# Kernel tuning notes

Hardware: AMD Instinct MI355X
Metric: run time of the kernel (lower is better)

Reference implementation:

```python
import jax, jax.numpy as jnp
import numpy as np


def _prelu(y, a):
    # nn.PReLU() with a single learned slope parameter
    return jnp.where(y >= 0, y, a * y)


def _proj1x1(x, w, b, a):
    # 1x1 conv: [N,C,H,W] x [O,C] -> [N,O,H,W], then bias + PReLU
    y = jnp.einsum('nchw,oc->nohw', x, w) + b[None, :, None, None]
    return _prelu(y, a)


def setup_inputs() -> dict:
    key = jax.random.key(0)
    ks = jax.random.split(key, 10)
    C, RC = 128, 64
    x = jax.random.normal(ks[0], (2, C, 96, 96), dtype=jnp.float32)
    s1 = 1.0 / np.sqrt(C)
    w1 = jax.random.normal(ks[1], (RC, C), dtype=jnp.float32) * s1
    b1 = jax.random.normal(ks[2], (RC,), dtype=jnp.float32) * 0.01
    a1 = jnp.full((1,), 0.25, dtype=jnp.float32)
    w2 = jax.random.normal(ks[3], (RC, C), dtype=jnp.float32) * s1
    b2 = jax.random.normal(ks[4], (RC,), dtype=jnp.float32) * 0.01
    a2 = jnp.full((1,), 0.25, dtype=jnp.float32)
    wa = jax.random.normal(ks[5], (C, C), dtype=jnp.float32) * s1
    ba = jax.random.normal(ks[6], (C,), dtype=jnp.float32) * 0.01
    aa = jnp.full((1,), 0.25, dtype=jnp.float32)
    return {"x": x, "w1": w1, "b1": b1, "a1": a1,
            "w2": w2, "b2": b2, "a2": a2,
            "wa": wa, "ba": ba, "aa": aa}


def reference(x, w1, b1, a1, w2, b2, a2, wa, ba, aa):
    N, C, H, W = x.shape
    HW = H * W
    # [N, rc, HW]
    x_embed_1 = _proj1x1(x, w1, b1, a1).reshape(N, -1, HW)
    # [N, HW, rc]
    x_embed_2 = _proj1x1(x, w2, b2, a2).reshape(N, -1, HW).transpose(0, 2, 1)
    # [N, C, HW]
    x_assembly = _proj1x1(x, wa, ba, aa).reshape(N, -1, HW)
    # [N, HW, HW]; NOTE: no 1/sqrt(d) scaling, softmax over dim=1 (faithful to torch)
    score = jax.nn.softmax(jnp.einsum('nqc,ncK->nqK', x_embed_2, x_embed_1), axis=1)
    out = jnp.einsum('ncq,nqK->ncK', x_assembly, score)
    return out.reshape(N, C, H, W)
```

## Files before the change

kernel.cpp:

```cpp
#include <hip/hip_runtime.h>

#define HWp 9216
#define CD 128
#define RC 64
#define NB 2
#define KSPLIT 4
#define NSTEPS 72
#define LOG2E 1.4426950408889634f

#define E2F_NSTR 589824
#define AVF_NSTR 1179648

typedef short s16x8 __attribute__((ext_vector_type(8)));
typedef unsigned short u16x8 __attribute__((ext_vector_type(8)));
typedef float fx4 __attribute__((ext_vector_type(4)));

__device__ __forceinline__ unsigned short f2bf(float f) {
    union { float f; unsigned int u; } cv; cv.f = f;
    unsigned int u = cv.u;
    u += 0x7FFFu + ((u >> 16) & 1u);
    return (unsigned short)(u >> 16);
}

__device__ __forceinline__ float fexp2(float x) {
    float r; asm("v_exp_f32 %0, %1" : "=v"(r) : "v"(x)); return r;
}

__device__ __forceinline__ unsigned int cvt_pk_bf16(float lo, float hi) {
    unsigned int r; asm("v_cvt_pk_bf16_f32 %0, %1, %2" : "=v"(r) : "v"(lo), "v"(hi)); return r;
}

__device__ __forceinline__ const float* uniform_ptr(const float* p) {
    unsigned long long v = (unsigned long long)(uintptr_t)p;
    unsigned int lo = __builtin_amdgcn_readfirstlane((unsigned int)v);
    unsigned int hi = __builtin_amdgcn_readfirstlane((unsigned int)(v >> 32));
    return (const float*)(uintptr_t)(((unsigned long long)hi << 32) | lo);
}

__global__ __launch_bounds__(256) void proj_kernel(
    const float* __restrict__ x,
    const float* __restrict__ w1, const float* __restrict__ b1, const float* __restrict__ a1,
    const float* __restrict__ w2, const float* __restrict__ b2, const float* __restrict__ a2,
    const float* __restrict__ wa, const float* __restrict__ ba, const float* __restrict__ aa,
    unsigned short* __restrict__ e1, unsigned short* __restrict__ e2f,
    unsigned short* __restrict__ avf)
{
    const int n = blockIdx.y;
    const int p0 = blockIdx.x * 64;
    const int wv = threadIdx.x >> 6;
    const int lane = threadIdx.x & 63;
    const int p = p0 + lane;
    const int row0 = blockIdx.z * 32 + wv * 8;
    const float* __restrict__ xb = x + (size_t)n * CD * HWp;

    const float* W; const float* B; const float* A; int r0; int mode; float oscale = 1.0f;
    if (row0 < 64)       { W = w1; B = b1; A = a1; r0 = row0;       mode = 0; oscale = LOG2E; }
    else if (row0 < 128) { W = w2; B = b2; A = a2; r0 = row0 - 64;  mode = 1; }
    else                 { W = wa; B = ba; A = aa; r0 = row0 - 128; mode = 2; }
    W = uniform_ptr(W); B = uniform_ptr(B);
    const float slope = A[0];

    float acc[8];
#pragma unroll
    for (int j = 0; j < 8; ++j) acc[j] = B[r0 + j];

    float xr[2][32];
#pragma unroll
    for (int i = 0; i < 32; ++i) xr[0][i] = xb[(size_t)i * HWp + p];
#pragma unroll
    for (int cc = 0; cc < 4; ++cc) {
        const int cur = cc & 1;
        if (cc < 3) {
#pragma unroll
            for (int i = 0; i < 32; ++i)
                xr[cur ^ 1][i] = xb[(size_t)((cc + 1) * 32 + i) * HWp + p];
        }
#pragma unroll
        for (int j = 0; j < 8; ++j) {
            const float* Wr = W + (size_t)(r0 + j) * CD + cc * 32;
            float a = acc[j];
#pragma unroll
            for (int i = 0; i < 32; ++i) a = __builtin_fmaf(Wr[i], xr[cur][i], a);
            acc[j] = a;
        }
    }
#pragma unroll
    for (int j = 0; j < 8; ++j) {
        float v = acc[j];
        acc[j] = (v >= 0.f ? v : slope * v) * oscale;
    }
    if (mode == 0) {
        u16x8 s0;
#pragma unroll
        for (int j = 0; j < 8; ++j) s0[j] = f2bf(acc[j]);
        unsigned short* dst = e1 + ((size_t)n * HWp + p) * RC + r0;
        *(u16x8*)(dst) = s0;
    } else if (mode == 1) {
        u16x8 s0;
#pragma unroll
        for (int j = 0; j < 8; ++j) s0[j] = f2bf(acc[j]);
        const int kb = p >> 5, kk = p & 31;
        const int l15w = ((kk >> 3) << 2) | (kk & 3);
        const int hw = (kk >> 2) & 1;
        const int ch = r0 >> 5;
        const int gA = (r0 >> 3) & 3;
        unsigned short* dst = e2f + (size_t)n * E2F_NSTR
                            + ((size_t)((kb * 4 + hw * 2 + ch) * 64 + gA * 16 + l15w)) * 8;
        *(u16x8*)(dst) = s0;
    } else {
        const int kb = p >> 5, gw = (p >> 3) & 3, jj = p & 7;
        const int ct = r0 >> 4;
        const int lbase = r0 & 15;
        unsigned short* base = avf + (size_t)n * AVF_NSTR
                             + ((size_t)((kb * 8 + ct) * 64 + gw * 16)) * 8 + jj;
#pragma unroll
        for (int j = 0; j < 8; ++j)
            base[(lbase + j) * 8] = f2bf(acc[j]);
    }
}

__global__ __launch_bounds__(256, 1) void attn_kernel(
    const unsigned short* __restrict__ e1,
    const unsigned short* __restrict__ e2f,
    const unsigned short* __restrict__ avf,
    float* __restrict__ out)
{
    const int wv = threadIdx.x >> 6;
    const int lane = threadIdx.x & 63;
    const int g = lane >> 4;
    const int l15 = lane & 15;

    const int bid = blockIdx.x;
    const int xcd = bid & 7;
    const int n = xcd >> 2;
    const int qslot = (xcd & 3) * 72 + (bid >> 3);
    const int qb = qslot * 32;

    const unsigned short* __restrict__ E1 = e1 + (size_t)n * HWp * RC;
    const unsigned short* __restrict__ E2F = e2f + (size_t)n * E2F_NSTR;
    const unsigned short* __restrict__ AVF = avf + (size_t)n * AVF_NSTR;

    s16x8 qf[2][2];
#pragma unroll
    for (int qc = 0; qc < 2; ++qc)
#pragma unroll
        for (int ch = 0; ch < 2; ++ch)
            qf[qc][ch] = *(const s16x8*)(E1 + ((size_t)(qb + qc * 16 + l15)) * RC + ch * 32 + g * 8);

    s16x8 ones;
#pragma unroll
    for (int j = 0; j < 8; ++j) ones[j] = (short)0x3F80;

    fx4 oacc[2][8];
    fx4 lacc[2];
#pragma unroll
    for (int qc = 0; qc < 2; ++qc) {
        lacc[qc] = (fx4){0.f, 0.f, 0.f, 0.f};
#pragma unroll
        for (int ct = 0; ct < 8; ++ct) oacc[qc][ct] = (fx4){0.f, 0.f, 0.f, 0.f};
    }

    const int kb0 = wv * NSTEPS;

    const unsigned short* kfp = E2F + (size_t)kb0 * 2048 + (size_t)lane * 8;
    const unsigned short* afp = AVF + (size_t)kb0 * 4096 + (size_t)lane * 8;

    s16x8 kfc[2][2];
#pragma unroll
    for (int h = 0; h < 2; ++h)
#pragma unroll
        for (int ch = 0; ch < 2; ++ch)
            kfc[h][ch] = *(const s16x8*)(kfp + (h * 2 + ch) * 512);
    kfp += 2048;

    union { s16x8 v; unsigned int w[4]; } pf[2];

    for (int kt = 0; kt < NSTEPS; ++kt) {
        s16x8 af[8];
#pragma unroll
        for (int ct = 0; ct < 8; ++ct)
            af[ct] = *(const s16x8*)(afp + ct * 512);
        afp += 4096;

        const unsigned short* kfsrc = (kt + 1 < NSTEPS) ? kfp : (kfp - 2048);
        s16x8 kfn[2][2];
#pragma unroll
        for (int h = 0; h < 2; ++h)
#pragma unroll
            for (int ch = 0; ch < 2; ++ch)
                kfn[h][ch] = *(const s16x8*)(kfsrc + (h * 2 + ch) * 512);
        kfp += 2048;

        fx4 s[2][2];
#pragma unroll
        for (int qc = 0; qc < 2; ++qc)
#pragma unroll
            for (int h = 0; h < 2; ++h) {
                fx4 a = (fx4){0.f, 0.f, 0.f, 0.f};
                a = __builtin_amdgcn_mfma_f32_16x16x32_bf16(kfc[h][0], qf[qc][0], a, 0, 0, 0);
                a = __builtin_amdgcn_mfma_f32_16x16x32_bf16(kfc[h][1], qf[qc][1], a, 0, 0, 0);
                s[qc][h] = a;
            }

#pragma unroll
        for (int qc = 0; qc < 2; ++qc) {
            float p0 = fexp2(s[qc][0][0]);
            float p1 = fexp2(s[qc][0][1]);
            float p2 = fexp2(s[qc][0][2]);
            float p3 = fexp2(s[qc][0][3]);
            float p4 = fexp2(s[qc][1][0]);
            float p5 = fexp2(s[qc][1][1]);
            float p6 = fexp2(s[qc][1][2]);
            float p7 = fexp2(s[qc][1][3]);
            pf[qc].w[0] = cvt_pk_bf16(p0, p1);
            pf[qc].w[1] = cvt_pk_bf16(p2, p3);
            pf[qc].w[2] = cvt_pk_bf16(p4, p5);
            pf[qc].w[3] = cvt_pk_bf16(p6, p7);
            lacc[qc] = __builtin_amdgcn_mfma_f32_16x16x32_bf16(ones, pf[qc].v, lacc[qc], 0, 0, 0);
        }

#pragma unroll
        for (int ct = 0; ct < 8; ++ct) {
            oacc[0][ct] = __builtin_amdgcn_mfma_f32_16x16x32_bf16(af[ct], pf[0].v, oacc[0][ct], 0, 0, 0);
            oacc[1][ct] = __builtin_amdgcn_mfma_f32_16x16x32_bf16(af[ct], pf[1].v, oacc[1][ct], 0, 0, 0);
        }

#pragma unroll
        for (int h = 0; h < 2; ++h)
#pragma unroll
            for (int ch = 0; ch < 2; ++ch)
                kfc[h][ch] = kfn[h][ch];
    }

    __shared__ float OA[32][CD + 4];
    __shared__ float LL[KSPLIT][32];
    __shared__ float LG[32];

    if (g == 0) {
#pragma unroll
        for (int qc = 0; qc < 2; ++qc)
            LL[wv][qc * 16 + l15] = lacc[qc][0];
    }
    __syncthreads();
    if (threadIdx.x < 32) {
        int q = threadIdx.x;
        float ls = 0.f;
#pragma unroll
        for (int w = 0; w < KSPLIT; ++w) ls += LL[w][q];
        LG[q] = ls;
    }
    for (int w = 0; w < KSPLIT; ++w) {
        if (wv == w) {
#pragma unroll
            for (int qc = 0; qc < 2; ++qc)
#pragma unroll
                for (int ct = 0; ct < 8; ++ct)
#pragma unroll
                    for (int r = 0; r < 4; ++r) {
                        int q = qc * 16 + l15;
                        int c = ct * 16 + g * 4 + r;
                        float v = oacc[qc][ct][r];
                        if (w == 0) OA[q][c] = v; else OA[q][c] += v;
                    }
        }
        __syncthreads();
    }
    {
        const int c = threadIdx.x >> 1;
        const int qh = (threadIdx.x & 1) * 16;
        float* __restrict__ dst = out + ((size_t)n * CD + c) * HWp + qb + qh;
#pragma unroll
        for (int j = 0; j < 16; ++j) dst[j] = OA[qh + j][c] / LG[qh + j];
    }
}

extern "C" void kernel_launch(void* const* d_in, const int* in_sizes, int n_in,
                              void* d_out, int out_size, void* d_ws, size_t ws_size,
                              hipStream_t stream) {
    const float* x  = (const float*)d_in[0];
    const float* w1 = (const float*)d_in[1];
    const float* b1 = (const float*)d_in[2];
    const float* a1 = (const float*)d_in[3];
    const float* w2 = (const float*)d_in[4];
    const float* b2 = (const float*)d_in[5];
    const float* a2 = (const float*)d_in[6];
    const float* wa = (const float*)d_in[7];
    const float* ba = (const float*)d_in[8];
    const float* aa = (const float*)d_in[9];
    float* out = (float*)d_out;

    char* ws = (char*)d_ws;
    unsigned short* e1  = (unsigned short*)ws;
    unsigned short* e2f = (unsigned short*)(ws + 2359296);
    unsigned short* avf = (unsigned short*)(ws + 4718592);

    dim3 pg(HWp / 64, NB, 8);
    proj_kernel<<<pg, 256, 0, stream>>>(x, w1, b1, a1, w2, b2, a2, wa, ba, aa, e1, e2f, avf);
    attn_kernel<<<dim3(576), 256, 0, stream>>>(e1, e2f, avf, out);
}
```

Measured before the change: 199.9 us.

## Retile attention blocks to 64 queries by half the channels

Each attention block now covers 64 queries and 64 output channels (a channel-group index is derived from the XCD id) instead of 32 queries and all 128 channels. The same number of value-tile loads now feeds twice as many query tiles, but the QK^T and exp work is duplicated across the two channel groups. Shared memory tiles and the output write mapping are resized to match. The projection kernel also drops its double-buffered x register prefetch for a simpler per-chunk load, which lowers register pressure.

```diff
diff --git a/kernel.cpp b/kernel.cpp
--- a/kernel.cpp
+++ b/kernel.cpp
@@ -63,24 +63,16 @@
     float acc[8];
 #pragma unroll
     for (int j = 0; j < 8; ++j) acc[j] = B[r0 + j];
-
-    float xr[2][32];
-#pragma unroll
-    for (int i = 0; i < 32; ++i) xr[0][i] = xb[(size_t)i * HWp + p];
-#pragma unroll
     for (int cc = 0; cc < 4; ++cc) {
-        const int cur = cc & 1;
-        if (cc < 3) {
-#pragma unroll
-            for (int i = 0; i < 32; ++i)
-                xr[cur ^ 1][i] = xb[(size_t)((cc + 1) * 32 + i) * HWp + p];
-        }
+        float xr[32];
+#pragma unroll
+        for (int i = 0; i < 32; ++i) xr[i] = xb[(size_t)(cc * 32 + i) * HWp + p];
 #pragma unroll
         for (int j = 0; j < 8; ++j) {
             const float* Wr = W + (size_t)(r0 + j) * CD + cc * 32;
             float a = acc[j];
 #pragma unroll
-            for (int i = 0; i < 32; ++i) a = __builtin_fmaf(Wr[i], xr[cur][i], a);
+            for (int i = 0; i < 32; ++i) a = __builtin_fmaf(Wr[i], xr[i], a);
             acc[j] = a;
         }
     }
@@ -133,16 +125,18 @@
     const int bid = blockIdx.x;
     const int xcd = bid & 7;
     const int n = xcd >> 2;
-    const int qslot = (xcd & 3) * 72 + (bid >> 3);
-    const int qb = qslot * 32;
+    const int cg = (xcd >> 1) & 1;
+    const int sub = xcd & 1;
+    const int qslot = (bid >> 3) * 2 + sub;
+    const int qb = qslot * 64;
 
     const unsigned short* __restrict__ E1 = e1 + (size_t)n * HWp * RC;
     const unsigned short* __restrict__ E2F = e2f + (size_t)n * E2F_NSTR;
     const unsigned short* __restrict__ AVF = avf + (size_t)n * AVF_NSTR;
 
-    s16x8 qf[2][2];
-#pragma unroll
-    for (int qc = 0; qc < 2; ++qc)
+    s16x8 qf[4][2];
+#pragma unroll
+    for (int qc = 0; qc < 4; ++qc)
 #pragma unroll
         for (int ch = 0; ch < 2; ++ch)
             qf[qc][ch] = *(const s16x8*)(E1 + ((size_t)(qb + qc * 16 + l15)) * RC + ch * 32 + g * 8);
@@ -151,19 +145,19 @@
 #pragma unroll
     for (int j = 0; j < 8; ++j) ones[j] = (short)0x3F80;
 
-    fx4 oacc[2][8];
-    fx4 lacc[2];
-#pragma unroll
-    for (int qc = 0; qc < 2; ++qc) {
+    fx4 oacc[4][4];
+    fx4 lacc[4];
+#pragma unroll
+    for (int qc = 0; qc < 4; ++qc) {
         lacc[qc] = (fx4){0.f, 0.f, 0.f, 0.f};
 #pragma unroll
-        for (int ct = 0; ct < 8; ++ct) oacc[qc][ct] = (fx4){0.f, 0.f, 0.f, 0.f};
+        for (int ct = 0; ct < 4; ++ct) oacc[qc][ct] = (fx4){0.f, 0.f, 0.f, 0.f};
     }
 
     const int kb0 = wv * NSTEPS;
 
     const unsigned short* kfp = E2F + (size_t)kb0 * 2048 + (size_t)lane * 8;
-    const unsigned short* afp = AVF + (size_t)kb0 * 4096 + (size_t)lane * 8;
+    const unsigned short* afp = AVF + (size_t)kb0 * 4096 + (size_t)(cg * 4) * 512 + (size_t)lane * 8;
 
     s16x8 kfc[2][2];
 #pragma unroll
@@ -173,12 +167,12 @@
             kfc[h][ch] = *(const s16x8*)(kfp + (h * 2 + ch) * 512);
     kfp += 2048;
 
-    union { s16x8 v; unsigned int w[4]; } pf[2];
+    union { s16x8 v; unsigned int w[4]; } pf[4];
 
     for (int kt = 0; kt < NSTEPS; ++kt) {
-        s16x8 af[8];
-#pragma unroll
-        for (int ct = 0; ct < 8; ++ct)
+        s16x8 af[4];
+#pragma unroll
+        for (int ct = 0; ct < 4; ++ct)
             af[ct] = *(const s16x8*)(afp + ct * 512);
         afp += 4096;
 
@@ -191,27 +185,22 @@
                 kfn[h][ch] = *(const s16x8*)(kfsrc + (h * 2 + ch) * 512);
         kfp += 2048;
 
-        fx4 s[2][2];
-#pragma unroll
-        for (int qc = 0; qc < 2; ++qc)
-#pragma unroll
-            for (int h = 0; h < 2; ++h) {
-                fx4 a = (fx4){0.f, 0.f, 0.f, 0.f};
-                a = __builtin_amdgcn_mfma_f32_16x16x32_bf16(kfc[h][0], qf[qc][0], a, 0, 0, 0);
-                a = __builtin_amdgcn_mfma_f32_16x16x32_bf16(kfc[h][1], qf[qc][1], a, 0, 0, 0);
-                s[qc][h] = a;
-            }
-
-#pragma unroll
-        for (int qc = 0; qc < 2; ++qc) {
-            float p0 = fexp2(s[qc][0][0]);
-            float p1 = fexp2(s[qc][0][1]);
-            float p2 = fexp2(s[qc][0][2]);
-            float p3 = fexp2(s[qc][0][3]);
-            float p4 = fexp2(s[qc][1][0]);
-            float p5 = fexp2(s[qc][1][1]);
-            float p6 = fexp2(s[qc][1][2]);
-            float p7 = fexp2(s[qc][1][3]);
+#pragma unroll
+        for (int qc = 0; qc < 4; ++qc) {
+            fx4 s0 = (fx4){0.f, 0.f, 0.f, 0.f};
+            fx4 s1 = (fx4){0.f, 0.f, 0.f, 0.f};
+            s0 = __builtin_amdgcn_mfma_f32_16x16x32_bf16(kfc[0][0], qf[qc][0], s0, 0, 0, 0);
+            s0 = __builtin_amdgcn_mfma_f32_16x16x32_bf16(kfc[0][1], qf[qc][1], s0, 0, 0, 0);
+            s1 = __builtin_amdgcn_mfma_f32_16x16x32_bf16(kfc[1][0], qf[qc][0], s1, 0, 0, 0);
+            s1 = __builtin_amdgcn_mfma_f32_16x16x32_bf16(kfc[1][1], qf[qc][1], s1, 0, 0, 0);
+            float p0 = fexp2(s0[0]);
+            float p1 = fexp2(s0[1]);
+            float p2 = fexp2(s0[2]);
+            float p3 = fexp2(s0[3]);
+            float p4 = fexp2(s1[0]);
+            float p5 = fexp2(s1[1]);
+            float p6 = fexp2(s1[2]);
+            float p7 = fexp2(s1[3]);
             pf[qc].w[0] = cvt_pk_bf16(p0, p1);
             pf[qc].w[1] = cvt_pk_bf16(p2, p3);
             pf[qc].w[2] = cvt_pk_bf16(p4, p5);
@@ -220,9 +209,11 @@
         }
 
 #pragma unroll
-        for (int ct = 0; ct < 8; ++ct) {
+        for (int ct = 0; ct < 4; ++ct) {
             oacc[0][ct] = __builtin_amdgcn_mfma_f32_16x16x32_bf16(af[ct], pf[0].v, oacc[0][ct], 0, 0, 0);
             oacc[1][ct] = __builtin_amdgcn_mfma_f32_16x16x32_bf16(af[ct], pf[1].v, oacc[1][ct], 0, 0, 0);
+            oacc[2][ct] = __builtin_amdgcn_mfma_f32_16x16x32_bf16(af[ct], pf[2].v, oacc[2][ct], 0, 0, 0);
+            oacc[3][ct] = __builtin_amdgcn_mfma_f32_16x16x32_bf16(af[ct], pf[3].v, oacc[3][ct], 0, 0, 0);
         }
 
 #pragma unroll
@@ -232,17 +223,17 @@
                 kfc[h][ch] = kfn[h][ch];
     }
 
-    __shared__ float OA[32][CD + 4];
-    __shared__ float LL[KSPLIT][32];
-    __shared__ float LG[32];
+    __shared__ float OA[64][68];
+    __shared__ float LL[KSPLIT][64];
+    __shared__ float LG[64];
 
     if (g == 0) {
 #pragma unroll
-        for (int qc = 0; qc < 2; ++qc)
+        for (int qc = 0; qc < 4; ++qc)
             LL[wv][qc * 16 + l15] = lacc[qc][0];
     }
     __syncthreads();
-    if (threadIdx.x < 32) {
+    if (threadIdx.x < 64) {
         int q = threadIdx.x;
         float ls = 0.f;
 #pragma unroll
@@ -252,9 +243,9 @@
     for (int w = 0; w < KSPLIT; ++w) {
         if (wv == w) {
 #pragma unroll
-            for (int qc = 0; qc < 2; ++qc)
-#pragma unroll
-                for (int ct = 0; ct < 8; ++ct)
+            for (int qc = 0; qc < 4; ++qc)
+#pragma unroll
+                for (int ct = 0; ct < 4; ++ct)
 #pragma unroll
                     for (int r = 0; r < 4; ++r) {
                         int q = qc * 16 + l15;
@@ -266,11 +257,11 @@
         __syncthreads();
     }
     {
-        const int c = threadIdx.x >> 1;
-        const int qh = (threadIdx.x & 1) * 16;
-        float* __restrict__ dst = out + ((size_t)n * CD + c) * HWp + qb + qh;
-#pragma unroll
-        for (int j = 0; j < 16; ++j) dst[j] = OA[qh + j][c] / LG[qh + j];
+        const int cl = threadIdx.x >> 2;
+        const int qh = (threadIdx.x & 3) * 16;
+        float* __restrict__ dst = out + ((size_t)n * CD + cg * 64 + cl) * HWp + qb + qh;
+#pragma unroll
+        for (int j = 0; j < 16; ++j) dst[j] = OA[qh + j][cl] / LG[qh + j];
     }
 }
 
```

New measurement: 212.1 us. +6.1%, slower.
